# Performance work log

Hardware: AMD Instinct MI355X
Metric: run time of the kernel (lower is better)

The kernel has to match this reference:

```python
import jax, jax.numpy as jnp
import numpy as np

DIM = 512
NUM_HEADS = 8
HEAD_DIM = DIM // NUM_HEADS
SCALE = HEAD_DIM ** -0.5


def setup_inputs() -> dict:
    key = jax.random.key(0)
    kx, kqw, kqb, kpw, kpb = jax.random.split(key, 5)
    B, N = 2, 4096
    x = jax.random.normal(kx, (B, N, DIM), dtype=jnp.float32)
    # nn.Linear weights stored as [out, in]; init ~ U(-1/sqrt(in), 1/sqrt(in))
    bound = 1.0 / np.sqrt(DIM)
    qkv_w = jax.random.uniform(kqw, (3 * DIM, DIM), minval=-bound, maxval=bound, dtype=jnp.float32)
    qkv_b = jax.random.uniform(kqb, (3 * DIM,), minval=-bound, maxval=bound, dtype=jnp.float32)
    proj_w = jax.random.uniform(kpw, (DIM, DIM), minval=-bound, maxval=bound, dtype=jnp.float32)
    proj_b = jax.random.uniform(kpb, (DIM,), minval=-bound, maxval=bound, dtype=jnp.float32)
    return {"x": x, "qkv_w": qkv_w, "qkv_b": qkv_b, "proj_w": proj_w, "proj_b": proj_b}


def reference(x, qkv_w, qkv_b, proj_w, proj_b):
    B, N, C = x.shape
    # qkv: [B, N, 3C] -> [3, B, H, N, Dh]
    qkv = x @ qkv_w.T + qkv_b
    qkv = qkv.reshape(B, N, 3, NUM_HEADS, HEAD_DIM).transpose(2, 0, 3, 1, 4)
    q, k, v = qkv[0], qkv[1], qkv[2]
    # scores: [B, H, N, N] (materialized, matching the original math)
    attn = jnp.einsum("bhqd,bhkd->bhqk", q, k) * SCALE
    attn = jax.nn.softmax(attn, axis=-1)
    out = jnp.einsum("bhqk,bhkd->bhqd", attn, v)  # [B, H, N, Dh]
    out = out.transpose(0, 2, 1, 3).reshape(B, N, C)
    return out @ proj_w.T + proj_b
```

## Files before the change

### kernel.cpp

```cpp
#include <hip/hip_runtime.h>
#include <hip/hip_bf16.h>
#include <stdint.h>
#include <stddef.h>

typedef __attribute__((ext_vector_type(8))) short short8;
typedef __attribute__((ext_vector_type(4))) float f32x4;
typedef __attribute__((ext_vector_type(16))) float f32x16;

#define MFMA16(a, b, c) __builtin_amdgcn_mfma_f32_16x16x32_bf16((a), (b), (c), 0, 0, 0)
#define MFMA32(a, b, c) __builtin_amdgcn_mfma_f32_32x32x16_bf16((a), (b), (c), 0, 0, 0)

#define QSCALE 0.1803368801111204f

#if __has_builtin(__builtin_amdgcn_exp2f)
#define EXP2(x) __builtin_amdgcn_exp2f(x)
#else
#define EXP2(x) __builtin_exp2f(x)
#endif

__device__ __forceinline__ float b2f(short x) {
    unsigned u = ((unsigned)(unsigned short)x) << 16;
    float f; __builtin_memcpy(&f, &u, 4); return f;
}
__device__ __forceinline__ short f2b(float f) {
    unsigned u; __builtin_memcpy(&u, &f, 4);
    u = (u + 0x7FFFu + ((u >> 16) & 1u)) >> 16;
    return (short)u;
}
__device__ __forceinline__ unsigned pack2(float a, float b) {
    unsigned ua, ub; __builtin_memcpy(&ua, &a, 4); __builtin_memcpy(&ub, &b, 4);
    return __builtin_amdgcn_perm(ub + 0x8000u, ua + 0x8000u, 0x07060302u);
}
__device__ __forceinline__ short8 load8f(const float* p) {
    const float4 f0 = *(const float4*)p;
    const float4 f1 = *(const float4*)(p + 4);
    short8 r;
    r[0]=f2b(f0.x); r[1]=f2b(f0.y); r[2]=f2b(f0.z); r[3]=f2b(f0.w);
    r[4]=f2b(f1.x); r[5]=f2b(f1.y); r[6]=f2b(f1.z); r[7]=f2b(f1.w);
    return r;
}

__global__ __launch_bounds__(256) void cvt3(
    const float* __restrict__ s0, short* __restrict__ d0, int n0,
    const float* __restrict__ s1, short* __restrict__ d1, int n1,
    const float* __restrict__ s2, short* __restrict__ d2, int n2)
{
    int i = blockIdx.x * 256 + threadIdx.x;
    if (i < n0) { *(short8*)(d0 + (size_t)i * 8) = load8f(s0 + (size_t)i * 8); return; }
    i -= n0;
    if (i < n1) { *(short8*)(d1 + (size_t)i * 8) = load8f(s1 + (size_t)i * 8); return; }
    i -= n1;
    if (i < n2) { *(short8*)(d2 + (size_t)i * 8) = load8f(s2 + (size_t)i * 8); }
}

__global__ __launch_bounds__(256) void qkv_gemm(
    const short* __restrict__ X, const short* __restrict__ W,
    const float* __restrict__ bias,
    short* __restrict__ Qb, short* __restrict__ Kb, short* __restrict__ Vb)
{
    __shared__ short sT[128][132];

    const int tid  = threadIdx.x;
    const int wv   = tid >> 6;
    const int lane = tid & 63;
    const int l15  = lane & 15;
    const int quad = lane >> 4;
    const int m0   = blockIdx.x * 128 + (wv >> 1) * 64;
    const int sec  = blockIdx.y >> 2;
    const int bis  = blockIdx.y & 3;
    const int nbase = sec * 512 + bis * 128;
    const int j0   = (wv & 1) * 64;

    const f32x4 zero = {0.f, 0.f, 0.f, 0.f};
    f32x4 acc[4][4];
#pragma unroll
    for (int i = 0; i < 4; i++)
#pragma unroll
        for (int j = 0; j < 4; j++) acc[i][j] = zero;

    for (int k0 = 0; k0 < 512; k0 += 32) {
        short8 a[4], b[4];
#pragma unroll
        for (int i = 0; i < 4; i++)
            a[i] = *(const short8*)(X + (size_t)(m0 + i * 16 + l15) * 512 + k0 + quad * 8);
#pragma unroll
        for (int j = 0; j < 4; j++)
            b[j] = *(const short8*)(W + (size_t)(nbase + j0 + j * 16 + l15) * 512 + k0 + quad * 8);
#pragma unroll
        for (int i = 0; i < 4; i++)
#pragma unroll
            for (int j = 0; j < 4; j++)
                acc[i][j] = MFMA16(a[i], b[j], acc[i][j]);
    }

    if (sec < 2) {
        const float scale = (sec == 0) ? QSCALE : 1.0f;
        short* dst = (sec == 0) ? Qb : Kb;
#pragma unroll
        for (int j = 0; j < 4; j++) {
            const int jc = bis * 128 + j0 + j * 16 + l15;
            const float bs = bias[sec * 512 + jc];
            const int hl = jc >> 6, d = jc & 63;
#pragma unroll
            for (int i = 0; i < 4; i++) {
#pragma unroll
                for (int r = 0; r < 4; r++) {
                    const int m = m0 + i * 16 + quad * 4 + r;
                    const int bb = m >> 12, seq = m & 4095;
                    dst[((size_t)(bb * 8 + hl) * 4096 + seq) * 64 + d] =
                        f2b((acc[i][j][r] + bs) * scale);
                }
            }
        }
    } else {
#pragma unroll
        for (int j = 0; j < 4; j++) {
            const int jcl = j0 + j * 16 + l15;
            const float bs = bias[nbase + jcl];
#pragma unroll
            for (int i = 0; i < 4; i++) {
                uint2 w;
                w.x = pack2(acc[i][j][0] + bs, acc[i][j][1] + bs);
                w.y = pack2(acc[i][j][2] + bs, acc[i][j][3] + bs);
                *(uint2*)&sT[jcl][(wv >> 1) * 64 + i * 16 + quad * 4] = w;
            }
        }
        __syncthreads();

        const int jcl = tid >> 1, half = tid & 1;
        const int hl = (bis * 128 + jcl) >> 6;
        const int d  = jcl & 63;
        const int bb = (blockIdx.x * 128) >> 12;
        const int seq0 = ((blockIdx.x * 128) & 4095) + half * 64;
        short* dst = Vb + ((size_t)(bb * 8 + hl) * 64 + d) * 4096 + seq0;
#pragma unroll
        for (int u = 0; u < 8; u++)
            *(short8*)(dst + u * 8) = *(const short8*)&sT[jcl][half * 64 + u * 8];
    }
}

__global__ __launch_bounds__(512, 4) void flash_attn(
    const short* __restrict__ Q, const short* __restrict__ K,
    const short* __restrict__ V, short* __restrict__ PO0,
    short* __restrict__ PO1, float* __restrict__ lbuf, int niter)
{
    __shared__ short sK[2][128][72];
    __shared__ short sV[2][64][136];

    const int tid  = threadIdx.x;
    const int wv   = tid >> 6;
    const int lane = tid & 63;
    const int l31  = lane & 31;
    const int half = lane >> 5;
    const int bh = blockIdx.y;
    const int b = bh >> 3, h = bh & 7;
    const int qw = blockIdx.x * 256 + wv * 32;
    const int ks = blockIdx.z;
    const int key0 = ks * niter * 128;

    const short* Qb = Q + (size_t)bh * 4096 * 64;
    const short* Kb = K + (size_t)bh * 4096 * 64;
    const short* Vb = V + (size_t)bh * 64 * 4096;

    short8 aq[4];
#pragma unroll
    for (int s = 0; s < 4; s++)
        aq[s] = *(const short8*)(Qb + (size_t)(qw + l31) * 64 + s * 16 + half * 8);

    short8 ones;
#pragma unroll
    for (int j = 0; j < 8; j++) ones[j] = (short)0x3F80;

    f32x16 o0 = {}, o1 = {};
    f32x16 o2 = {};

    const int r0  = tid >> 3;
    const int scb = (tid & 7) * 8;
    const int vb  = (scb & ~12) | ((scb & 8) >> 1);

    short8 pk0, pk1, pv0, pv1;
    pk0 = *(const short8*)(Kb + (size_t)(key0 + r0) * 64 + scb);
    pk1 = *(const short8*)(Kb + (size_t)(key0 + 64 + r0) * 64 + scb);
    pv0 = *(const short8*)(Vb + (size_t)r0 * 4096 + key0 + scb);
    pv1 = *(const short8*)(Vb + (size_t)r0 * 4096 + key0 + 64 + scb);
    *(short8*)&sK[0][r0][scb]      = pk0;
    *(short8*)&sK[0][64 + r0][scb] = pk1;
    *(uint2*)&sV[0][r0][vb]          = ((const uint2*)&pv0)[0];
    *(uint2*)&sV[0][r0][vb + 8]      = ((const uint2*)&pv0)[1];
    *(uint2*)&sV[0][64 + vb]         = ((const uint2*)&pv1)[0];
    *(uint2*)&sV[0][r0][64 + vb]     = ((const uint2*)&pv1)[0];
    *(uint2*)&sV[0][r0][64 + vb + 8] = ((const uint2*)&pv1)[1];
    {
        const int kn = key0 + 128;
        pk0 = *(const short8*)(Kb + (size_t)(kn + r0) * 64 + scb);
        pk1 = *(const short8*)(Kb + (size_t)(kn + 64 + r0) * 64 + scb);
        pv0 = *(const short8*)(Vb + (size_t)r0 * 4096 + kn + scb);
        pv1 = *(const short8*)(Vb + (size_t)r0 * 4096 + kn + 64 + scb);
    }

    for (int kt = 0; kt < niter; ++kt) {
        __syncthreads();

        if (kt + 1 < niter) {
            short (*sKn)[72]  = sK[(kt + 1) & 1];
            short (*sVn)[136] = sV[(kt + 1) & 1];
            *(short8*)&sKn[r0][scb]      = pk0;
            *(short8*)&sKn[64 + r0][scb] = pk1;
            *(uint2*)&sVn[r0][vb]          = ((const uint2*)&pv0)[0];
            *(uint2*)&sVn[r0][vb + 8]      = ((const uint2*)&pv0)[1];
            *(uint2*)&sVn[r0][64 + vb]     = ((const uint2*)&pv1)[0];
            *(uint2*)&sVn[r0][64 + vb + 8] = ((const uint2*)&pv1)[1];
        }
        if (kt + 2 < niter) {
            const int kn = key0 + (kt + 2) * 128;
            pk0 = *(const short8*)(Kb + (size_t)(kn + r0) * 64 + scb);
            pk1 = *(const short8*)(Kb + (size_t)(kn + 64 + r0) * 64 + scb);
            pv0 = *(const short8*)(Vb + (size_t)r0 * 4096 + kn + scb);
            pv1 = *(const short8*)(Vb + (size_t)r0 * 4096 + kn + 64 + scb);
        }

        const short (*sKc)[72]  = sK[kt & 1];
        const short (*sVc)[136] = sV[kt & 1];

#pragma unroll
        for (int c = 0; c < 4; c++) {
            f32x16 ST = {};
            __builtin_amdgcn_s_setprio(1);
#pragma unroll
            for (int s = 0; s < 4; s++) {
                const short8 bk = *(const short8*)&sKc[c * 32 + l31][s * 16 + half * 8];
                ST = MFMA32(bk, aq[s], ST);
            }
            __builtin_amdgcn_s_setprio(0);
            float e[16];
#pragma unroll
            for (int r = 0; r < 16; r++) e[r] = EXP2(ST[r]);
            uint4 w0 = { pack2(e[0], e[1]),  pack2(e[2], e[3]),
                         pack2(e[4], e[5]),  pack2(e[6], e[7]) };
            uint4 w1 = { pack2(e[8], e[9]),  pack2(e[10], e[11]),
                         pack2(e[12], e[13]), pack2(e[14], e[15]) };
            const short8 bp0 = *(const short8*)&w0;
            const short8 bp1 = *(const short8*)&w1;

            __builtin_amdgcn_s_setprio(1);
            const short8 bv00 = *(const short8*)&sVc[l31][(2 * c) * 16 + half * 8];
            const short8 bv01 = *(const short8*)&sVc[32 + l31][(2 * c) * 16 + half * 8];
            o0 = MFMA32(bv00, bp0, o0);
            o1 = MFMA32(bv01, bp0, o1);
            o2 = MFMA32(ones, bp0, o2);
            const short8 bv10 = *(const short8*)&sVc[l31][(2 * c + 1) * 16 + half * 8];
            const short8 bv11 = *(const short8*)&sVc[32 + l31][(2 * c + 1) * 16 + half * 8];
            o0 = MFMA32(bv10, bp1, o0);
            o1 = MFMA32(bv11, bp1, o1);
            o2 = MFMA32(ones, bp1, o2);
            __builtin_amdgcn_s_setprio(0);
        }
    }

    const float lsum = o2[0];
    const float inv = 1.f / fmaxf(lsum, 1e-30f);

    short* PO = (ks == 0) ? PO0 : PO1;
#pragma unroll
    for (int q = 0; q < 4; q++) {
        uint2 w0, w1;
        w0.x = pack2(o0[4 * q + 0] * inv, o0[4 * q + 1] * inv);
        w0.y = pack2(o0[4 * q + 2] * inv, o0[4 * q + 3] * inv);
        w1.x = pack2(o1[4 * q + 0] * inv, o1[4 * q + 1] * inv);
        w1.y = pack2(o1[4 * q + 2] * inv, o1[4 * q + 3] * inv);
        const size_t rowoff = ((size_t)b * 4096 + qw + l31) * 512;
        const int col = h * 64 + q * 8 + half * 4;
        *(uint2*)(PO + rowoff + col) = w0;
        *(uint2*)(PO + rowoff + col + 32) = w1;
    }
    if (half == 0)
        lbuf[((size_t)ks * 16 + bh) * 4096 + qw + l31] = lsum;
}

__global__ __launch_bounds__(256) void combine(
    const short* __restrict__ PO0, const short* __restrict__ PO1,
    short* __restrict__ attn, const float* __restrict__ L)
{
    const int i = blockIdx.x * 256 + threadIdx.x;
    const size_t flat = (size_t)i * 8;
    const int col = (int)(flat & 511);
    const int q   = (int)((flat >> 9) & 4095);
    const int b   = (int)(flat >> 21);
    const int bh  = b * 8 + (col >> 6);
    const float l0 = L[(size_t)bh * 4096 + q];
    const float l1 = L[(size_t)65536 + (size_t)bh * 4096 + q];
    const float inv = 1.f / (l0 + l1);
    const float w0 = l0 * inv, w1 = l1 * inv;
    const short8 a = *(const short8*)(PO0 + flat);
    const short8 c = *(const short8*)(PO1 + flat);
    short8 r;
#pragma unroll
    for (int k = 0; k < 8; k += 2) {
        const unsigned p = pack2(w0 * b2f(a[k]) + w1 * b2f(c[k]),
                                 w0 * b2f(a[k + 1]) + w1 * b2f(c[k + 1]));
        r[k]     = (short)(p & 0xFFFF);
        r[k + 1] = (short)(p >> 16);
    }
    *(short8*)(attn + flat) = r;
}

__global__ __launch_bounds__(256) void proj_gemm(
    const short* __restrict__ A, const short* __restrict__ W,
    const float* __restrict__ bias, float* __restrict__ dst)
{
    const int tid  = threadIdx.x;
    const int wv   = tid >> 6;
    const int lane = tid & 63;
    const int l15  = lane & 15;
    const int quad = lane >> 4;
    const int m0 = blockIdx.x * 128 + (wv >> 1) * 64;
    const int n0 = blockIdx.y * 128 + (wv & 1) * 64;

    const f32x4 zero = {0.f, 0.f, 0.f, 0.f};
    f32x4 acc[4][4];
#pragma unroll
    for (int i = 0; i < 4; i++)
#pragma unroll
        for (int j = 0; j < 4; j++) acc[i][j] = zero;

    for (int k0 = 0; k0 < 512; k0 += 32) {
        short8 a[4], b[4];
#pragma unroll
        for (int i = 0; i < 4; i++)
            a[i] = *(const short8*)(A + (size_t)(m0 + i * 16 + l15) * 512 + k0 + quad * 8);
#pragma unroll
        for (int j = 0; j < 4; j++)
            b[j] = *(const short8*)(W + (size_t)(n0 + j * 16 + l15) * 512 + k0 + quad * 8);
#pragma unroll
        for (int i = 0; i < 4; i++)
#pragma unroll
            for (int j = 0; j < 4; j++)
                acc[i][j] = MFMA16(a[i], b[j], acc[i][j]);
    }

#pragma unroll
    for (int j = 0; j < 4; j++) {
        const int n = n0 + j * 16 + l15;
        const float bs = bias[n];
#pragma unroll
        for (int i = 0; i < 4; i++) {
#pragma unroll
            for (int r = 0; r < 4; r++) {
                const int m = m0 + i * 16 + quad * 4 + r;
                dst[(size_t)m * 512 + n] = acc[i][j][r] + bs;
            }
        }
    }
}

extern "C" void kernel_launch(void* const* d_in, const int* in_sizes, int n_in,
                              void* d_out, int out_size, void* d_ws, size_t ws_size,
                              hipStream_t stream)
{
    const float* x      = (const float*)d_in[0];
    const float* qkv_w  = (const float*)d_in[1];
    const float* qkv_b  = (const float*)d_in[2];
    const float* proj_w = (const float*)d_in[3];
    const float* proj_b = (const float*)d_in[4];

    const size_t MB = 1024 * 1024;
    short* xb   = (short*)d_out;
    short* wb   = (short*)d_out + 4 * MB;
    short* PO0  = (short*)d_out;
    short* PO1  = (short*)d_out + 4 * MB;
    float* out  = (float*)d_out;

    short* Qf = (short*)d_ws;
    short* Kf = Qf + (size_t)16 * 4096 * 64;
    short* Vf = Kf + (size_t)16 * 4096 * 64;
    short* attn = Qf;
    float* lbuf = (float*)((char*)d_ws + 24 * MB);
    short* pwb  = (short*)((char*)d_ws + 24 * MB + 512 * 1024);

    cvt3<<<2560, 256, 0, stream>>>(x, xb, 524288, qkv_w, wb, 98304, proj_w, pwb, 32768);
    qkv_gemm<<<dim3(64, 12), 256, 0, stream>>>(xb, wb, qkv_b, Qf, Kf, Vf);
    flash_attn<<<dim3(16, 16, 2), 512, 0, stream>>>(Qf, Kf, Vf, PO0, PO1, lbuf, 16);
    combine<<<2048, 256, 0, stream>>>(PO0, PO1, attn, lbuf);
    proj_gemm<<<dim3(64, 4), 256, 0, stream>>>(attn, pwb, proj_b, out);
}
```

Before: 241.3 us.

## Software-pipeline QK and PV tiles, sum softmax denominators in VALU, use cvt_pk_bf16

```diff
diff --git a/kernel.cpp b/kernel.cpp
--- a/kernel.cpp
+++ b/kernel.cpp
@@ -30,6 +30,11 @@
 __device__ __forceinline__ unsigned pack2(float a, float b) {
     unsigned ua, ub; __builtin_memcpy(&ua, &a, 4); __builtin_memcpy(&ub, &b, 4);
     return __builtin_amdgcn_perm(ub + 0x8000u, ua + 0x8000u, 0x07060302u);
+}
+__device__ __forceinline__ unsigned cvtpk(float a, float b) {
+    unsigned r;
+    asm("v_cvt_pk_bf16_f32 %0, %1, %2" : "=v"(r) : "v"(a), "v"(b));
+    return r;
 }
 __device__ __forceinline__ short8 load8f(const float* p) {
     const float4 f0 = *(const float4*)p;
@@ -139,6 +144,51 @@
     }
 }
 
+__device__ __forceinline__ f32x16 qk_tile(const short (*sKc)[72], int c,
+                                          int l31, int half, const short8* aq)
+{
+    f32x16 st = {};
+    __builtin_amdgcn_s_setprio(1);
+#pragma unroll
+    for (int s = 0; s < 4; s++) {
+        const short8 bk = *(const short8*)&sKc[c * 32 + l31][s * 16 + half * 8];
+        st = MFMA32(bk, aq[s], st);
+    }
+    __builtin_amdgcn_s_setprio(0);
+    return st;
+}
+
+__device__ __forceinline__ void pv_tile(const short (*sVc)[136], int c,
+                                        int l31, int half, const f32x16& st,
+                                        f32x16& o0, f32x16& o1,
+                                        float& la0, float& la1, float& la2, float& la3)
+{
+    float e[16];
+#pragma unroll
+    for (int r = 0; r < 16; r++) e[r] = EXP2(st[r]);
+    la0 += (e[0] + e[1]) + (e[2] + e[3]);
+    la1 += (e[4] + e[5]) + (e[6] + e[7]);
+    la2 += (e[8] + e[9]) + (e[10] + e[11]);
+    la3 += (e[12] + e[13]) + (e[14] + e[15]);
+    uint4 w0 = { cvtpk(e[0], e[1]),   cvtpk(e[2], e[3]),
+                 cvtpk(e[4], e[5]),   cvtpk(e[6], e[7]) };
+    uint4 w1 = { cvtpk(e[8], e[9]),   cvtpk(e[10], e[11]),
+                 cvtpk(e[12], e[13]), cvtpk(e[14], e[15]) };
+    const short8 bp0 = *(const short8*)&w0;
+    const short8 bp1 = *(const short8*)&w1;
+
+    __builtin_amdgcn_s_setprio(1);
+    const short8 bv00 = *(const short8*)&sVc[l31][(2 * c) * 16 + half * 8];
+    const short8 bv01 = *(const short8*)&sVc[32 + l31][(2 * c) * 16 + half * 8];
+    o0 = MFMA32(bv00, bp0, o0);
+    o1 = MFMA32(bv01, bp0, o1);
+    const short8 bv10 = *(const short8*)&sVc[l31][(2 * c + 1) * 16 + half * 8];
+    const short8 bv11 = *(const short8*)&sVc[32 + l31][(2 * c + 1) * 16 + half * 8];
+    o0 = MFMA32(bv10, bp1, o0);
+    o1 = MFMA32(bv11, bp1, o1);
+    __builtin_amdgcn_s_setprio(0);
+}
+
 __global__ __launch_bounds__(512, 4) void flash_attn(
     const short* __restrict__ Q, const short* __restrict__ K,
     const short* __restrict__ V, short* __restrict__ PO0,
@@ -167,12 +217,8 @@
     for (int s = 0; s < 4; s++)
         aq[s] = *(const short8*)(Qb + (size_t)(qw + l31) * 64 + s * 16 + half * 8);
 
-    short8 ones;
-#pragma unroll
-    for (int j = 0; j < 8; j++) ones[j] = (short)0x3F80;
-
     f32x16 o0 = {}, o1 = {};
-    f32x16 o2 = {};
+    float la0 = 0.f, la1 = 0.f, la2 = 0.f, la3 = 0.f;
 
     const int r0  = tid >> 3;
     const int scb = (tid & 7) * 8;
@@ -187,7 +233,6 @@
     *(short8*)&sK[0][64 + r0][scb] = pk1;
     *(uint2*)&sV[0][r0][vb]          = ((const uint2*)&pv0)[0];
     *(uint2*)&sV[0][r0][vb + 8]      = ((const uint2*)&pv0)[1];
-    *(uint2*)&sV[0][64 + vb]         = ((const uint2*)&pv1)[0];
     *(uint2*)&sV[0][r0][64 + vb]     = ((const uint2*)&pv1)[0];
     *(uint2*)&sV[0][r0][64 + vb + 8] = ((const uint2*)&pv1)[1];
     {
@@ -222,42 +267,18 @@
         const short (*sKc)[72]  = sK[kt & 1];
         const short (*sVc)[136] = sV[kt & 1];
 
-#pragma unroll
-        for (int c = 0; c < 4; c++) {
-            f32x16 ST = {};
-            __builtin_amdgcn_s_setprio(1);
-#pragma unroll
-            for (int s = 0; s < 4; s++) {
-                const short8 bk = *(const short8*)&sKc[c * 32 + l31][s * 16 + half * 8];
-                ST = MFMA32(bk, aq[s], ST);
-            }
-            __builtin_amdgcn_s_setprio(0);
-            float e[16];
-#pragma unroll
-            for (int r = 0; r < 16; r++) e[r] = EXP2(ST[r]);
-            uint4 w0 = { pack2(e[0], e[1]),  pack2(e[2], e[3]),
-                         pack2(e[4], e[5]),  pack2(e[6], e[7]) };
-            uint4 w1 = { pack2(e[8], e[9]),  pack2(e[10], e[11]),
-                         pack2(e[12], e[13]), pack2(e[14], e[15]) };
-            const short8 bp0 = *(const short8*)&w0;
-            const short8 bp1 = *(const short8*)&w1;
-
-            __builtin_amdgcn_s_setprio(1);
-            const short8 bv00 = *(const short8*)&sVc[l31][(2 * c) * 16 + half * 8];
-            const short8 bv01 = *(const short8*)&sVc[32 + l31][(2 * c) * 16 + half * 8];
-            o0 = MFMA32(bv00, bp0, o0);
-            o1 = MFMA32(bv01, bp0, o1);
-            o2 = MFMA32(ones, bp0, o2);
-            const short8 bv10 = *(const short8*)&sVc[l31][(2 * c + 1) * 16 + half * 8];
-            const short8 bv11 = *(const short8*)&sVc[32 + l31][(2 * c + 1) * 16 + half * 8];
-            o0 = MFMA32(bv10, bp1, o0);
-            o1 = MFMA32(bv11, bp1, o1);
-            o2 = MFMA32(ones, bp1, o2);
-            __builtin_amdgcn_s_setprio(0);
-        }
-    }
-
-    const float lsum = o2[0];
+        f32x16 stA = qk_tile(sKc, 0, l31, half, aq);
+        f32x16 stB = qk_tile(sKc, 1, l31, half, aq);
+        pv_tile(sVc, 0, l31, half, stA, o0, o1, la0, la1, la2, la3);
+        stA = qk_tile(sKc, 2, l31, half, aq);
+        pv_tile(sVc, 1, l31, half, stB, o0, o1, la0, la1, la2, la3);
+        stB = qk_tile(sKc, 3, l31, half, aq);
+        pv_tile(sVc, 2, l31, half, stA, o0, o1, la0, la1, la2, la3);
+        pv_tile(sVc, 3, l31, half, stB, o0, o1, la0, la1, la2, la3);
+    }
+
+    float lsum = (la0 + la1) + (la2 + la3);
+    lsum += __shfl_xor(lsum, 32);
     const float inv = 1.f / fmaxf(lsum, 1e-30f);
 
     short* PO = (ks == 0) ? PO0 : PO1;
```

Result: slower. 249.9 us (+3.6%).
